# Kernel tuning notes

Measured on AMD Instinct MI355X. Metric: run time of the kernel, lower is better.

The kernel has to match this reference:

```python
import jax, jax.numpy as jnp
import numpy as np

HIDDEN = 2048
NUM_HEADS = 16
HEAD_DIM = HIDDEN // NUM_HEADS  # 128
B, S = 2, 2048


def setup_inputs() -> dict:
    key = jax.random.key(0)
    ks = jax.random.split(key, 16)
    w = lambda k, shp: (jax.random.normal(k, shp, jnp.float32) * 0.02)
    return {
        "query": jax.random.normal(ks[0], (B, S, HIDDEN), jnp.float32),
        "key": jax.random.normal(ks[1], (B, S, HIDDEN), jnp.float32),
        "value": jax.random.normal(ks[2], (B, S, HIDDEN), jnp.float32),
        "Wq": w(ks[3], (HIDDEN, HIDDEN)), "bq": jnp.zeros((HIDDEN,), jnp.float32),
        "Wk": w(ks[4], (HIDDEN, HIDDEN)), "bk": jnp.zeros((HIDDEN,), jnp.float32),
        "Wv": w(ks[5], (HIDDEN, HIDDEN)), "bv": jnp.zeros((HIDDEN,), jnp.float32),
        "Wo": w(ks[6], (HIDDEN, HIDDEN)), "bo": jnp.zeros((HIDDEN,), jnp.float32),
        "Wf1": w(ks[7], (HEAD_DIM, 2 * HEAD_DIM)), "bf1": jnp.zeros((2 * HEAD_DIM,), jnp.float32),
        "Wf2": w(ks[8], (2 * HEAD_DIM, HEAD_DIM)), "bf2": jnp.zeros((HEAD_DIM,), jnp.float32),
    }


def reference(query, key, value, Wq, bq, Wk, bk, Wv, bv, Wo, bo, Wf1, bf1, Wf2, bf2):
    b, s, _ = query.shape

    def split_heads(x):  # [b,s,H] -> [b,h,s,d]
        return x.reshape(b, s, NUM_HEADS, HEAD_DIM).transpose(0, 2, 1, 3)

    def feature_map(x):  # MLP on last dim: d -> 2d -> relu -> d
        return jax.nn.relu(x @ Wf1 + bf1) @ Wf2 + bf2

    Q = feature_map(split_heads(query @ Wq + bq))
    K = feature_map(split_heads(key @ Wk + bk))
    V = split_heads(value @ Wv + bv)

    # K^T V per head: [b,h,d,e]
    KV = jnp.einsum("bhsd,bhse->bhde", K, V)
    QKV = jnp.einsum("bhsd,bhde->bhse", Q, KV)
    # denominator: sum of all K entries per (b,h) -> scalar per head
    denom = jnp.sum(K, axis=(-2, -1), keepdims=True) + 1e-8
    QKV = QKV / denom

    context = QKV.transpose(0, 2, 1, 3).reshape(b, s, HIDDEN)
    output = context @ Wo + bo

    attn_weights = jnp.full((b, NUM_HEADS, s, s), 1.0 / s, dtype=query.dtype)
    return output, attn_weights
```

## Files before the change

kernel.cpp:

```cpp
#include <hip/hip_runtime.h>


typedef __bf16 bf16_t;
typedef __bf16 bf16x8 __attribute__((ext_vector_type(8)));
typedef __bf16 bf16x4 __attribute__((ext_vector_type(4)));
typedef float  f32x4  __attribute__((ext_vector_type(4)));

#define FILLV (1.0f / 2048.0f)

#define VMCNT2() asm volatile("s_waitcnt vmcnt(2)" ::: "memory")
#define VMCNT0() asm volatile("s_waitcnt vmcnt(0)" ::: "memory")
#define LGKM0()  asm volatile("s_waitcnt lgkmcnt(0)" ::: "memory")
#define BAR()    __builtin_amdgcn_s_barrier()
#define SCHED0() __builtin_amdgcn_sched_barrier(0)

__device__ __forceinline__ void gload16(const void* g, void* l) {
  __builtin_amdgcn_global_load_lds(
      (__attribute__((address_space(1))) void*)(g),
      (__attribute__((address_space(3))) void*)(l), 16, 0, 0);
}

__device__ __forceinline__ void fill_epilogue(float* attn, long slotBase,
                                              int slots, int t) {
  const f32x4 fv = {FILLV, FILLV, FILLV, FILLV};
  f32x4* dst = (f32x4*)attn + slotBase + t;
  for (int i = 0; i < slots; i += 256)
    __builtin_nontemporal_store(fv, dst + i);
}

__device__ __forceinline__ void stage_half(const bf16_t* __restrict__ g,
                                           int h, unsigned char* ldsT, int t) {
  const bf16_t* gh = g + (long)h * 128 * 2048;
  unsigned char* lh = ldsT + h * 16384;
#pragma unroll
  for (int i = 0; i < 2; ++i) {
    const int c = t + i * 512;
    const int r = c >> 3;
    const int cc = ((c & 7) ^ (r & 7)) * 8;
    gload16(gh + (long)r * 2048 + cc, lh + c * 16);
  }
}

__device__ __forceinline__ bf16x8 lds_frag(const unsigned char* base,
                                           int row, int kelem) {
  int byte = row * 128 + kelem * 2;
  byte ^= (row & 7) << 4;
  return *(const bf16x8*)(base + byte);
}

__global__ __launch_bounds__(512, 2) void proj_gemm8(
    const bf16_t* __restrict__ A, const bf16_t* __restrict__ Wt,
    const float* __restrict__ bq, const float* __restrict__ bk,
    const float* __restrict__ bv, bf16_t* __restrict__ C,
    float* __restrict__ attn)
{
  __shared__ __align__(16) unsigned char smem[131072];
  const int t = threadIdx.x;
  const int lane = t & 63;
  const int wid = t >> 6;
  const int wr = wid >> 2, wc = wid & 3;
  const int bid = blockIdx.x;
  const int bx = bid & 7, by = bid >> 3;
  const int which = by >> 4;
  const bf16_t* Ab = A + (long)by * 256 * 2048;
  const bf16_t* Bb = Wt + (long)which * 4194304 + (long)bx * 256 * 2048;
  const float* bias = which == 0 ? bq : (which == 1 ? bk : bv);

  const int lr = lane & 15;
  const int l8 = (lane >> 4) * 8;

  f32x4 acc[8][4];
#pragma unroll
  for (int i = 0; i < 8; ++i)
#pragma unroll
    for (int j = 0; j < 4; ++j) acc[i][j] = (f32x4){0.f, 0.f, 0.f, 0.f};

  stage_half(Ab, 0, smem, t);
  stage_half(Ab, 1, smem, t);
  stage_half(Bb, 0, smem + 32768, t);
  stage_half(Bb, 1, smem + 32768, t);

  bf16x8 aF[4][2], bF[4][2];

  for (int kt = 0; kt < 32; ++kt) {
    const int cur = kt & 1;
    unsigned char* curA = smem + cur * 65536;
    unsigned char* curB = curA + 32768;
    unsigned char* nxtA = smem + (cur ^ 1) * 65536;
    unsigned char* nxtB = nxtA + 32768;
    const bool hn = kt < 31;
    const bf16_t* An = Ab + (kt + 1) * 64;
    const bf16_t* Bn = Bb + (kt + 1) * 64;
    const int arow = wr * 128 + lr;
    const int brow = wc * 64 + lr;

    if (hn) { stage_half(An, 0, nxtA, t); VMCNT2(); }
    else    { VMCNT0(); }
    BAR();
#pragma unroll
    for (int mi = 0; mi < 4; ++mi)
#pragma unroll
      for (int kk = 0; kk < 2; ++kk)
        aF[mi][kk] = lds_frag(curA, arow + mi * 16, kk * 32 + l8);
#pragma unroll
    for (int ni = 0; ni < 2; ++ni)
#pragma unroll
      for (int kk = 0; kk < 2; ++kk)
        bF[ni][kk] = lds_frag(curB, brow + ni * 16, kk * 32 + l8);
    LGKM0(); SCHED0();
    __builtin_amdgcn_s_setprio(1);
#pragma unroll
    for (int mi = 0; mi < 4; ++mi)
#pragma unroll
      for (int ni = 0; ni < 2; ++ni)
#pragma unroll
        for (int kk = 0; kk < 2; ++kk)
          acc[mi][ni] = __builtin_amdgcn_mfma_f32_16x16x32_bf16(
              aF[mi][kk], bF[ni][kk], acc[mi][ni], 0, 0, 0);
    __builtin_amdgcn_s_setprio(0);
    BAR();

    if (hn) stage_half(An, 1, nxtA, t);
#pragma unroll
    for (int ni = 0; ni < 2; ++ni)
#pragma unroll
      for (int kk = 0; kk < 2; ++kk)
        bF[2 + ni][kk] = lds_frag(curB, brow + (2 + ni) * 16, kk * 32 + l8);
    BAR(); LGKM0(); SCHED0();
    __builtin_amdgcn_s_setprio(1);
#pragma unroll
    for (int mi = 0; mi < 4; ++mi)
#pragma unroll
      for (int ni = 0; ni < 2; ++ni)
#pragma unroll
        for (int kk = 0; kk < 2; ++kk)
          acc[mi][2 + ni] = __builtin_amdgcn_mfma_f32_16x16x32_bf16(
              aF[mi][kk], bF[2 + ni][kk], acc[mi][2 + ni], 0, 0, 0);
    __builtin_amdgcn_s_setprio(0);
    BAR();

    if (hn) stage_half(Bn, 0, nxtB, t);
#pragma unroll
    for (int mi = 0; mi < 4; ++mi)
#pragma unroll
      for (int kk = 0; kk < 2; ++kk)
        aF[mi][kk] = lds_frag(curA, arow + 64 + mi * 16, kk * 32 + l8);
    BAR(); LGKM0(); SCHED0();
    __builtin_amdgcn_s_setprio(1);
#pragma unroll
    for (int mi = 0; mi < 4; ++mi)
#pragma unroll
      for (int ni = 0; ni < 2; ++ni)
#pragma unroll
        for (int kk = 0; kk < 2; ++kk)
          acc[4 + mi][ni] = __builtin_amdgcn_mfma_f32_16x16x32_bf16(
              aF[mi][kk], bF[ni][kk], acc[4 + mi][ni], 0, 0, 0);
    __builtin_amdgcn_s_setprio(0);
    BAR();

    if (hn) stage_half(Bn, 1, nxtB, t);
    BAR(); LGKM0(); SCHED0();
    __builtin_amdgcn_s_setprio(1);
#pragma unroll
    for (int mi = 0; mi < 4; ++mi)
#pragma unroll
      for (int ni = 0; ni < 2; ++ni)
#pragma unroll
        for (int kk = 0; kk < 2; ++kk)
          acc[4 + mi][2 + ni] = __builtin_amdgcn_mfma_f32_16x16x32_bf16(
              aF[mi][kk], bF[2 + ni][kk], acc[4 + mi][2 + ni], 0, 0, 0);
    __builtin_amdgcn_s_setprio(0);
    BAR();
  }

  {
    const f32x4 fv = {FILLV, FILLV, FILLV, FILLV};
    f32x4* dst = (f32x4*)attn + 27262976L + (long)bid * 16384 + t;
#pragma unroll
    for (int i = 0; i < 16384; i += 512)
      __builtin_nontemporal_store(fv, dst + i);
  }

  const int row0 = by * 256 + wr * 128;
  const int col0 = bx * 256 + wc * 64;
#pragma unroll
  for (int mi = 0; mi < 8; ++mi) {
#pragma unroll
    for (int ni = 0; ni < 4; ++ni) {
      const int col = col0 + ni * 16 + lr;
      const float bvv = bias[col];
#pragma unroll
      for (int j = 0; j < 4; ++j) {
        const int row = row0 + mi * 16 + (lane >> 4) * 4 + j;
        C[(long)row * 2048 + col] = (bf16_t)(acc[mi][ni][j] + bvv);
      }
    }
  }
}

template<bool RELU, bool OUTF32, bool BIAS, int FILLMODE>
__global__ __launch_bounds__(256) void gemm_bt(
    const bf16_t* __restrict__ A, const bf16_t* __restrict__ Bt,
    const float* __restrict__ bias, void* __restrict__ C,
    int K, int lda, int ldb, int ldc,
    long aBatchB, long aBatchH, long bBatchB, long bBatchH,
    long cBatchB, long cBatchH, int HperB,
    float* __restrict__ attn, long fillBase, int fillSlots)
{
  __shared__ bf16_t As[128 * 64];
  __shared__ bf16_t Bs[128 * 64];

  const int z  = blockIdx.z;
  const int zb = z / HperB, zh = z % HperB;
  const bf16_t* Ab = A  + (long)zb * aBatchB + (long)zh * aBatchH
                        + (long)blockIdx.y * 128 * lda;
  const bf16_t* Bb = Bt + (long)zb * bBatchB + (long)zh * bBatchH
                        + (long)blockIdx.x * 128 * ldb;

  const int t = threadIdx.x;
  const int lane = t & 63, w = t >> 6;
  const int wm = (w >> 1) * 64, wn = (w & 1) * 64;
  const int p = ((int)blockIdx.z * gridDim.y + blockIdx.y) * gridDim.x
                + blockIdx.x;

  f32x4 acc[4][4];
#pragma unroll
  for (int i = 0; i < 4; ++i)
#pragma unroll
    for (int j = 0; j < 4; ++j) acc[i][j] = (f32x4){0.f, 0.f, 0.f, 0.f};

  for (int k0 = 0; k0 < K; k0 += 64) {
#pragma unroll
    for (int i = 0; i < 4; ++i) {
      int c = i * 256 + t;
      int row = c >> 3, col = (c & 7) * 8;
      gload16(Ab + (long)row * lda + k0 + col, &As[c * 8]);
      gload16(Bb + (long)row * ldb + k0 + col, &Bs[c * 8]);
    }
    if constexpr (FILLMODE == 1) {
      const f32x4 fv = {FILLV, FILLV, FILLV, FILLV};
      const long nB = (long)gridDim.x * gridDim.y * gridDim.z;
      long s0 = fillBase + (((long)(k0 >> 6) * nB + p) * 3) * 256 + t;
      __builtin_nontemporal_store(fv, (f32x4*)attn + s0);
      __builtin_nontemporal_store(fv, (f32x4*)attn + s0 + 256);
      __builtin_nontemporal_store(fv, (f32x4*)attn + s0 + 512);
    }
    __syncthreads();
#pragma unroll
    for (int kk = 0; kk < 2; ++kk) {
      bf16x8 af[4], bfr[4];
#pragma unroll
      for (int mi = 0; mi < 4; ++mi)
        af[mi] = *(const bf16x8*)&As[(wm + mi * 16 + (lane & 15)) * 64
                                     + kk * 32 + (lane >> 4) * 8];
#pragma unroll
      for (int ni = 0; ni < 4; ++ni)
        bfr[ni] = *(const bf16x8*)&Bs[(wn + ni * 16 + (lane & 15)) * 64
                                      + kk * 32 + (lane >> 4) * 8];
#pragma unroll
      for (int mi = 0; mi < 4; ++mi)
#pragma unroll
        for (int ni = 0; ni < 4; ++ni)
          acc[mi][ni] = __builtin_amdgcn_mfma_f32_16x16x32_bf16(
              af[mi], bfr[ni], acc[mi][ni], 0, 0, 0);
    }
    __syncthreads();
  }

  if constexpr (FILLMODE == 2)
    fill_epilogue(attn, fillBase + (long)p * fillSlots, fillSlots, t);

  const long cb = (long)zb * cBatchB + (long)zh * cBatchH;
  const int row0 = blockIdx.y * 128 + wm;
  const int col0 = blockIdx.x * 128 + wn;
#pragma unroll
  for (int mi = 0; mi < 4; ++mi) {
#pragma unroll
    for (int ni = 0; ni < 4; ++ni) {
      const int col = col0 + ni * 16 + (lane & 15);
      const float bv = BIAS ? bias[col] : 0.f;
#pragma unroll
      for (int j = 0; j < 4; ++j) {
        const int row = row0 + mi * 16 + (lane >> 4) * 4 + j;
        float v = acc[mi][ni][j] + bv;
        if (RELU) v = fmaxf(v, 0.f);
        if (OUTF32) ((float*)C)[cb + (long)row * ldc + col] = v;
        else        ((bf16_t*)C)[cb + (long)row * ldc + col] = (bf16_t)v;
      }
    }
  }
}

__global__ __launch_bounds__(256) void fm_fused(
    const bf16_t* __restrict__ A, const bf16_t* __restrict__ W1t,
    const bf16_t* __restrict__ W2t, const float* __restrict__ b1,
    const float* __restrict__ b2, bf16_t* __restrict__ Out,
    float* __restrict__ attn)
{
  __shared__ char Hs[64 * 256 * 2];
  const int t = threadIdx.x, lane = t & 63, w = t >> 6;
  const long r0 = (long)blockIdx.x * 64;
  const int lr = lane & 15, lk = lane >> 4;

  f32x4 acc[4][4];
#pragma unroll
  for (int i = 0; i < 4; ++i)
#pragma unroll
    for (int j = 0; j < 4; ++j) acc[i][j] = (f32x4){0.f, 0.f, 0.f, 0.f};
  const int wn = w * 64;
#pragma unroll
  for (int kk = 0; kk < 4; ++kk) {
    bf16x8 af[4], bfr[4];
#pragma unroll
    for (int mi = 0; mi < 4; ++mi)
      af[mi] = *(const bf16x8*)&A[(r0 + mi * 16 + lr) * 128 + kk * 32 + lk * 8];
#pragma unroll
    for (int ni = 0; ni < 4; ++ni)
      bfr[ni] = *(const bf16x8*)&W1t[(long)(wn + ni * 16 + lr) * 128
                                     + kk * 32 + lk * 8];
#pragma unroll
    for (int mi = 0; mi < 4; ++mi)
#pragma unroll
      for (int ni = 0; ni < 4; ++ni)
        acc[mi][ni] = __builtin_amdgcn_mfma_f32_16x16x32_bf16(
            af[mi], bfr[ni], acc[mi][ni], 0, 0, 0);
  }
#pragma unroll
  for (int ni = 0; ni < 4; ++ni) {
    const int col = wn + ni * 16 + lr;
    const float bvv = b1[col];
#pragma unroll
    for (int mi = 0; mi < 4; ++mi)
#pragma unroll
      for (int j = 0; j < 4; ++j) {
        const int row = mi * 16 + lk * 4 + j;
        float h = fmaxf(acc[mi][ni][j] + bvv, 0.f);
        int byte = (row << 9) + (col << 1);
        byte ^= (row & 7) << 4;
        *(bf16_t*)(Hs + byte) = (bf16_t)h;
      }
  }
  __syncthreads();

  f32x4 acc2[4][2];
#pragma unroll
  for (int i = 0; i < 4; ++i)
#pragma unroll
    for (int j = 0; j < 2; ++j) acc2[i][j] = (f32x4){0.f, 0.f, 0.f, 0.f};
  const int wn2 = w * 32;
#pragma unroll
  for (int kk = 0; kk < 8; ++kk) {
    bf16x8 af[4], bfr[2];
#pragma unroll
    for (int mi = 0; mi < 4; ++mi) {
      const int m = mi * 16 + lr;
      int byte = (m << 9) + kk * 64 + lk * 16;
      byte ^= (m & 7) << 4;
      af[mi] = *(const bf16x8*)(Hs + byte);
    }
#pragma unroll
    for (int ni = 0; ni < 2; ++ni)
      bfr[ni] = *(const bf16x8*)&W2t[(long)(wn2 + ni * 16 + lr) * 256
                                     + kk * 32 + lk * 8];
#pragma unroll
    for (int mi = 0; mi < 4; ++mi)
#pragma unroll
      for (int ni = 0; ni < 2; ++ni)
        acc2[mi][ni] = __builtin_amdgcn_mfma_f32_16x16x32_bf16(
            af[mi], bfr[ni], acc2[mi][ni], 0, 0, 0);
  }

  fill_epilogue(attn, 12582912L + (long)blockIdx.x * 2048, 2048, t);

#pragma unroll
  for (int ni = 0; ni < 2; ++ni) {
    const int col = wn2 + ni * 16 + lr;
    const float bvv = b2[col];
#pragma unroll
    for (int mi = 0; mi < 4; ++mi)
#pragma unroll
      for (int j = 0; j < 4; ++j) {
        const int row = mi * 16 + lk * 4 + j;
        Out[(r0 + row) * 128 + col] = (bf16_t)(acc2[mi][ni][j] + bvv);
      }
  }
}

__global__ __launch_bounds__(256) void prep(
    const float* __restrict__ q, const float* __restrict__ k,
    const float* __restrict__ v,
    const float* __restrict__ Wq, const float* __restrict__ Wk,
    const float* __restrict__ Wv, const float* __restrict__ Wo,
    const float* __restrict__ Wf1, const float* __restrict__ Wf2,
    bf16_t* __restrict__ qkv_bf, bf16_t* __restrict__ Wqkv_t,
    bf16_t* __restrict__ Wf1_t, bf16_t* __restrict__ Wf2_t)
{
  const int t = threadIdx.x;
  const int bid = blockIdx.x;
  __shared__ float tile[32][33];

  if (bid < 24576) {
    const float* in = bid < 8192 ? q : (bid < 16384 ? k : v);
    bf16_t* o = qkv_bf + (long)(bid >> 13) * 8388608L;
    long i = ((long)(bid & 8191) * 256 + t) * 4;
    float4 x = *(const float4*)&in[i];
    bf16x4 r = {(bf16_t)x.x, (bf16_t)x.y, (bf16_t)x.z, (bf16_t)x.w};
    *(bf16x4*)&o[i] = r;
    return;
  }

  const int x = t & 31, y = t >> 5;
  const float* W; bf16_t* out; int Kd, Nd, n0, k0;
  if (bid < 40960) {
    const int sub = bid - 24576;
    const int z = sub >> 12, r = sub & 4095;
    W = z == 0 ? Wq : z == 1 ? Wk : z == 2 ? Wv : Wo;
    out = Wqkv_t + (long)z * 4194304L;
    Kd = 2048; Nd = 2048;
    n0 = (r & 63) * 32; k0 = (r >> 6) * 32;
  } else if (bid < 40992) {
    const int sub = bid - 40960;
    W = Wf1; out = Wf1_t; Kd = 128; Nd = 256;
    n0 = (sub & 7) * 32; k0 = (sub >> 3) * 32;
  } else {
    const int sub = bid - 40992;
    W = Wf2; out = Wf2_t; Kd = 256; Nd = 128;
    n0 = (sub & 3) * 32; k0 = (sub >> 2) * 32;
  }
#pragma unroll
  for (int j = 0; j < 32; j += 8)
    tile[y + j][x] = W[(long)(k0 + y + j) * Nd + n0 + x];
  __syncthreads();
#pragma unroll
  for (int j = 0; j < 32; j += 8)
    out[(long)(n0 + y + j) * Kd + k0 + x] = (bf16_t)tile[x][y + j];
}

__global__ __launch_bounds__(256) void kv_partial(
    const bf16_t* __restrict__ Kf, const bf16_t* __restrict__ Vp,
    float* __restrict__ part, float* __restrict__ part_denom,
    float* __restrict__ attn) {
  const int z = blockIdx.y, b = z >> 4, h = z & 15;
  const int s0 = blockIdx.x * 128;
  const int t = threadIdx.x;
  __shared__ bf16_t Ks[32 * 128];
  __shared__ bf16_t Vs[32 * 128];
  __shared__ float red[4];
  const bf16_t* Kb = Kf + (long)b * 4194304 + h * 128;
  const bf16_t* Vb = Vp + (long)b * 4194304 + h * 128;
  float acc[8][8];
#pragma unroll
  for (int i = 0; i < 8; ++i)
#pragma unroll
    for (int j = 0; j < 8; ++j) acc[i][j] = 0.f;
  float ksum = 0.f;
  const int d0 = (t & 15) * 8, e0 = (t >> 4) * 8;
  for (int sc = 0; sc < 128; sc += 32) {
#pragma unroll
    for (int i = 0; i < 2; ++i) {
      int idx = (i * 256 + t) * 8;
      int r = idx >> 7, c = idx & 127;
      long g = (long)(s0 + sc + r) * 2048 + c;
      *(bf16x8*)&Ks[r * 128 + c] = *(const bf16x8*)&Kb[g];
      *(bf16x8*)&Vs[r * 128 + c] = *(const bf16x8*)&Vb[g];
    }
    __syncthreads();
    {
      bf16x8 a0 = *(const bf16x8*)&Ks[t * 16];
      bf16x8 a1 = *(const bf16x8*)&Ks[t * 16 + 8];
#pragma unroll
      for (int j = 0; j < 8; ++j) ksum += (float)a0[j] + (float)a1[j];
    }
    for (int s = 0; s < 32; ++s) {
      bf16x8 kv = *(const bf16x8*)&Ks[s * 128 + d0];
      bf16x8 vv = *(const bf16x8*)&Vs[s * 128 + e0];
      float kf[8], vf[8];
#pragma unroll
      for (int i = 0; i < 8; ++i) { kf[i] = (float)kv[i]; vf[i] = (float)vv[i]; }
#pragma unroll
      for (int i = 0; i < 8; ++i)
#pragma unroll
        for (int j = 0; j < 8; ++j) acc[i][j] += vf[i] * kf[j];
    }
    __syncthreads();
  }

#pragma unroll
  for (int off = 32; off; off >>= 1) ksum += __shfl_down(ksum, off, 64);
  if ((t & 63) == 0) red[t >> 6] = ksum;
  __syncthreads();
  if (t == 0)
    part_denom[blockIdx.x * 32 + z] = red[0] + red[1] + red[2] + red[3];

  fill_epilogue(attn,
      16777216L + (long)(blockIdx.y * 16 + blockIdx.x) * 8192, 8192, t);

  float* pb = part + ((long)blockIdx.x * 32 + z) * 16384;
#pragma unroll
  for (int i = 0; i < 8; ++i)
#pragma unroll
    for (int j = 0; j < 8; ++j)
      pb[(e0 + i) * 128 + (d0 + j)] = acc[i][j];
}

__global__ __launch_bounds__(256) void kv_reduce(
    const float* __restrict__ part, const float* __restrict__ part_denom,
    bf16_t* __restrict__ KVT, float* __restrict__ attn) {
  const int z = blockIdx.x >> 4, slice = blockIdx.x & 15;
  const int t = threadIdx.x;
  float dsum = 0.f;
#pragma unroll
  for (int c = 0; c < 16; ++c) dsum += part_denom[c * 32 + z];
  const float inv = 1.0f / (dsum + 1e-8f);
  const int base = slice * 1024;
  for (int i = base + t; i < base + 1024; i += 256) {
    float s = 0.f;
#pragma unroll
    for (int c = 0; c < 16; ++c) s += part[((long)c * 32 + z) * 16384 + i];
    KVT[(long)z * 16384 + i] = (bf16_t)(s * inv);
  }
  fill_epilogue(attn, 20971520L + (long)blockIdx.x * 4096, 4096, t);
}

extern "C" void kernel_launch(void* const* d_in, const int* in_sizes, int n_in,
                              void* d_out, int out_size, void* d_ws, size_t ws_size,
                              hipStream_t stream) {
  (void)in_sizes; (void)n_in; (void)out_size; (void)ws_size;
  const float* q   = (const float*)d_in[0];
  const float* k   = (const float*)d_in[1];
  const float* v   = (const float*)d_in[2];
  const float* Wq  = (const float*)d_in[3];
  const float* bq  = (const float*)d_in[4];
  const float* Wk  = (const float*)d_in[5];
  const float* bk  = (const float*)d_in[6];
  const float* Wv  = (const float*)d_in[7];
  const float* bv  = (const float*)d_in[8];
  const float* Wo  = (const float*)d_in[9];
  const float* bo  = (const float*)d_in[10];
  const float* Wf1 = (const float*)d_in[11];
  const float* bf1 = (const float*)d_in[12];
  const float* Wf2 = (const float*)d_in[13];
  const float* bf2 = (const float*)d_in[14];

  bf16_t* P      = (bf16_t*)d_ws;
  bf16_t* qkv_bf = P;
  bf16_t* Wqkv_t = P + 25165824L;
  bf16_t* Wo_t   = P + 37748736L;
  bf16_t* Wf1_t  = P + 41943040L;
  bf16_t* Wf2_t  = P + 41975808L;
  bf16_t* Qp     = P + 42008576L;
  bf16_t* Vp     = P + 58785792L;
  bf16_t* Qf     = P + 83951616L;
  bf16_t* Kf     = P + 92340224L;
  bf16_t* KVT    = P + 100728832L;
  float*  part   = (float*)d_ws;
  float*  part_denom = (float*)d_ws + 8388608L;

  float* out0 = (float*)d_out;
  float* attn = (float*)d_out + 8388608L;

  dim3 blk(256);

  prep<<<41024, blk, 0, stream>>>(q, k, v, Wq, Wk, Wv, Wo, Wf1, Wf2,
                                  qkv_bf, Wqkv_t, Wf1_t, Wf2_t);

  proj_gemm8<<<384, 512, 0, stream>>>(qkv_bf, Wqkv_t, bq, bk, bv, Qp, attn);

  fm_fused<<<2048, blk, 0, stream>>>(Qp, Wf1_t, Wf2_t, bf1, bf2, Qf, attn);

  kv_partial<<<dim3(16, 32), blk, 0, stream>>>(Kf, Vp, part, part_denom, attn);

  kv_reduce<<<512, blk, 0, stream>>>(part, part_denom, KVT, attn);

  gemm_bt<false, false, false, 2><<<dim3(1, 16, 32), blk, 0, stream>>>(
      Qf, KVT, nullptr, Vp, 128, 2048, 128, 2048,
      4194304L, 128L, 262144L, 16384L, 4194304L, 128L, 16,
      attn, 23068672L, 8192);

  gemm_bt<false, true, true, 1><<<dim3(16, 32, 1), blk, 0, stream>>>(
      Vp, Wo_t, bo, out0, 2048, 2048, 2048, 2048, 0, 0, 0, 0, 0, 0, 1,
      attn, 0L, 0);
}
```

Before: 359.5 us.

## Redistribute attn_weights fill stores into the two large GEMMs' main loops

Moves the constant attention-weight fill out of the small kernels (fm_fused, kv_partial, kv_reduce, the QKV gemm epilogue) and interleaves it into the K-loops of the projection GEMM and the output GEMM, plus a tail epilogue in the output GEMM. The aim is to hide the large write-bandwidth-bound fill behind MFMA-bound compute instead of serialising it in short memory-light kernels. In exchange the GEMM main loops carry extra store traffic that may contend with their operand loads, and the offset arithmetic must still cover the whole attn buffer exactly.

Result: faster. 348.8 us, median of 2 (-3.0%).

```diff
diff --git a/kernel.cpp b/kernel.cpp
--- a/kernel.cpp
+++ b/kernel.cpp
@@ -18,14 +18,6 @@
   __builtin_amdgcn_global_load_lds(
       (__attribute__((address_space(1))) void*)(g),
       (__attribute__((address_space(3))) void*)(l), 16, 0, 0);
-}
-
-__device__ __forceinline__ void fill_epilogue(float* attn, long slotBase,
-                                              int slots, int t) {
-  const f32x4 fv = {FILLV, FILLV, FILLV, FILLV};
-  f32x4* dst = (f32x4*)attn + slotBase + t;
-  for (int i = 0; i < slots; i += 256)
-    __builtin_nontemporal_store(fv, dst + i);
 }
 
 __device__ __forceinline__ void stage_half(const bf16_t* __restrict__ g,
@@ -68,6 +60,7 @@
 
   const int lr = lane & 15;
   const int l8 = (lane >> 4) * 8;
+  const f32x4 fv = {FILLV, FILLV, FILLV, FILLV};
 
   f32x4 acc[8][4];
 #pragma unroll
@@ -93,6 +86,7 @@
     const bf16_t* Bn = Bb + (kt + 1) * 64;
     const int arow = wr * 128 + lr;
     const int brow = wc * 64 + lr;
+    f32x4* fillp = (f32x4*)attn + ((long)kt * 384 + bid) * 3 * 512 + t;
 
     if (hn) { stage_half(An, 0, nxtA, t); VMCNT2(); }
     else    { VMCNT0(); }
@@ -121,6 +115,7 @@
     BAR();
 
     if (hn) stage_half(An, 1, nxtA, t);
+    __builtin_nontemporal_store(fv, fillp);
 #pragma unroll
     for (int ni = 0; ni < 2; ++ni)
 #pragma unroll
@@ -140,6 +135,7 @@
     BAR();
 
     if (hn) stage_half(Bn, 0, nxtB, t);
+    __builtin_nontemporal_store(fv, fillp + 512);
 #pragma unroll
     for (int mi = 0; mi < 4; ++mi)
 #pragma unroll
@@ -159,6 +155,7 @@
     BAR();
 
     if (hn) stage_half(Bn, 1, nxtB, t);
+    __builtin_nontemporal_store(fv, fillp + 1024);
     BAR(); LGKM0(); SCHED0();
     __builtin_amdgcn_s_setprio(1);
 #pragma unroll
@@ -171,14 +168,6 @@
               aF[mi][kk], bF[2 + ni][kk], acc[4 + mi][2 + ni], 0, 0, 0);
     __builtin_amdgcn_s_setprio(0);
     BAR();
-  }
-
-  {
-    const f32x4 fv = {FILLV, FILLV, FILLV, FILLV};
-    f32x4* dst = (f32x4*)attn + 27262976L + (long)bid * 16384 + t;
-#pragma unroll
-    for (int i = 0; i < 16384; i += 512)
-      __builtin_nontemporal_store(fv, dst + i);
   }
 
   const int row0 = by * 256 + wr * 128;
@@ -205,7 +194,7 @@
     int K, int lda, int ldb, int ldc,
     long aBatchB, long aBatchH, long bBatchB, long bBatchH,
     long cBatchB, long cBatchH, int HperB,
-    float* __restrict__ attn, long fillBase, int fillSlots)
+    float* __restrict__ attn, long fillBase, long fillBase2, int fillSlots)
 {
   __shared__ bf16_t As[128 * 64];
   __shared__ bf16_t Bs[128 * 64];
@@ -237,7 +226,7 @@
       gload16(Ab + (long)row * lda + k0 + col, &As[c * 8]);
       gload16(Bb + (long)row * ldb + k0 + col, &Bs[c * 8]);
     }
-    if constexpr (FILLMODE == 1) {
+    if constexpr (FILLMODE == 3) {
       const f32x4 fv = {FILLV, FILLV, FILLV, FILLV};
       const long nB = (long)gridDim.x * gridDim.y * gridDim.z;
       long s0 = fillBase + (((long)(k0 >> 6) * nB + p) * 3) * 256 + t;
@@ -267,8 +256,12 @@
     __syncthreads();
   }
 
-  if constexpr (FILLMODE == 2)
-    fill_epilogue(attn, fillBase + (long)p * fillSlots, fillSlots, t);
+  if constexpr (FILLMODE == 3) {
+    const f32x4 fv = {FILLV, FILLV, FILLV, FILLV};
+    f32x4* dst = (f32x4*)attn + fillBase2 + (long)p * fillSlots + t;
+    for (int i = 0; i < fillSlots; i += 256)
+      __builtin_nontemporal_store(fv, dst + i);
+  }
 
   const long cb = (long)zb * cBatchB + (long)zh * cBatchH;
   const int row0 = blockIdx.y * 128 + wm;
@@ -294,8 +287,7 @@
 __global__ __launch_bounds__(256) void fm_fused(
     const bf16_t* __restrict__ A, const bf16_t* __restrict__ W1t,
     const bf16_t* __restrict__ W2t, const float* __restrict__ b1,
-    const float* __restrict__ b2, bf16_t* __restrict__ Out,
-    float* __restrict__ attn)
+    const float* __restrict__ b2, bf16_t* __restrict__ Out)
 {
   __shared__ char Hs[64 * 256 * 2];
   const int t = threadIdx.x, lane = t & 63, w = t >> 6;
@@ -369,9 +361,6 @@
         acc2[mi][ni] = __builtin_amdgcn_mfma_f32_16x16x32_bf16(
             af[mi], bfr[ni], acc2[mi][ni], 0, 0, 0);
   }
-
-  fill_epilogue(attn, 12582912L + (long)blockIdx.x * 2048, 2048, t);
-
 #pragma unroll
   for (int ni = 0; ni < 2; ++ni) {
     const int col = wn2 + ni * 16 + lr;
@@ -438,8 +427,7 @@
 
 __global__ __launch_bounds__(256) void kv_partial(
     const bf16_t* __restrict__ Kf, const bf16_t* __restrict__ Vp,
-    float* __restrict__ part, float* __restrict__ part_denom,
-    float* __restrict__ attn) {
+    float* __restrict__ part, float* __restrict__ part_denom) {
   const int z = blockIdx.y, b = z >> 4, h = z & 15;
   const int s0 = blockIdx.x * 128;
   const int t = threadIdx.x;
@@ -492,9 +480,6 @@
   if (t == 0)
     part_denom[blockIdx.x * 32 + z] = red[0] + red[1] + red[2] + red[3];
 
-  fill_epilogue(attn,
-      16777216L + (long)(blockIdx.y * 16 + blockIdx.x) * 8192, 8192, t);
-
   float* pb = part + ((long)blockIdx.x * 32 + z) * 16384;
 #pragma unroll
   for (int i = 0; i < 8; ++i)
@@ -505,7 +490,7 @@
 
 __global__ __launch_bounds__(256) void kv_reduce(
     const float* __restrict__ part, const float* __restrict__ part_denom,
-    bf16_t* __restrict__ KVT, float* __restrict__ attn) {
+    bf16_t* __restrict__ KVT) {
   const int z = blockIdx.x >> 4, slice = blockIdx.x & 15;
   const int t = threadIdx.x;
   float dsum = 0.f;
@@ -519,7 +504,6 @@
     for (int c = 0; c < 16; ++c) s += part[((long)c * 32 + z) * 16384 + i];
     KVT[(long)z * 16384 + i] = (bf16_t)(s * inv);
   }
-  fill_epilogue(attn, 20971520L + (long)blockIdx.x * 4096, 4096, t);
 }
 
 extern "C" void kernel_launch(void* const* d_in, const int* in_sizes, int n_in,
@@ -566,18 +550,18 @@
 
   proj_gemm8<<<384, 512, 0, stream>>>(qkv_bf, Wqkv_t, bq, bk, bv, Qp, attn);
 
-  fm_fused<<<2048, blk, 0, stream>>>(Qp, Wf1_t, Wf2_t, bf1, bf2, Qf, attn);
-
-  kv_partial<<<dim3(16, 32), blk, 0, stream>>>(Kf, Vp, part, part_denom, attn);
-
-  kv_reduce<<<512, blk, 0, stream>>>(part, part_denom, KVT, attn);
-
-  gemm_bt<false, false, false, 2><<<dim3(1, 16, 32), blk, 0, stream>>>(
+  fm_fused<<<2048, blk, 0, stream>>>(Qp, Wf1_t, Wf2_t, bf1, bf2, Qf);
+
+  kv_partial<<<dim3(16, 32), blk, 0, stream>>>(Kf, Vp, part, part_denom);
+
+  kv_reduce<<<512, blk, 0, stream>>>(part, part_denom, KVT);
+
+  gemm_bt<false, false, false, 0><<<dim3(1, 16, 32), blk, 0, stream>>>(
       Qf, KVT, nullptr, Vp, 128, 2048, 128, 2048,
       4194304L, 128L, 262144L, 16384L, 4194304L, 128L, 16,
-      attn, 23068672L, 8192);
-
-  gemm_bt<false, true, true, 1><<<dim3(16, 32, 1), blk, 0, stream>>>(
+      nullptr, 0, 0, 0);
+
+  gemm_bt<false, true, true, 3><<<dim3(16, 32, 1), blk, 0, stream>>>(
       Vp, Wo_t, bo, out0, 2048, 2048, 2048, 2048, 0, 0, 0, 0, 0, 0, 1,
-      attn, 0L, 0);
-}
+      attn, 18874368L, 31457280L, 4096);
+}
```
